# Optimization experiments

Hardware: AMD Instinct MI355X
Metric: run time of the kernel (lower is better)

## Reference

```python
import jax, jax.numpy as jnp
import numpy as np

B, H, S, D = 2, 16, 2048, 128

def setup_inputs() -> dict:
    key = jax.random.key(0)
    kq, kk, kv = jax.random.split(key, 3)
    q = jax.random.normal(kq, (B, H, S, D), dtype=jnp.float32)
    k = jax.random.normal(kk, (B, H, S, D), dtype=jnp.float32)
    v = jax.random.normal(kv, (B, H, S, D), dtype=jnp.float32)
    # causal mask, broadcastable over batch and heads; 0 -> masked out
    mask = jnp.tril(jnp.ones((S, S), dtype=jnp.int32))[None, None, :, :]
    return {"q": q, "k": k, "v": v, "mask": mask}

def reference(q, k, v, mask):
    # scores: [B,H,S,S] -- note: module applies NO 1/sqrt(d) scaling
    attn = jnp.einsum('bhqd,bhkd->bhqk', q, k)
    neg_inf = jnp.finfo(attn.dtype).min
    attn = jnp.where(mask == 0, neg_inf, attn)
    attn = jax.nn.softmax(attn, axis=-1)
    out = jnp.einsum('bhqk,bhkd->bhqd', attn, v)
    return out
```

## Files before the change

kernel.cpp:

```cpp
#include <hip/hip_runtime.h>


#define SQ 2048
#define DH 128
#define BM 64
#define BN 64
#define NELEM 8388608

typedef _Float16 f16x8 __attribute__((ext_vector_type(8)));
typedef float f32x4 __attribute__((ext_vector_type(4)));
typedef unsigned short u16x8 __attribute__((ext_vector_type(8)));

typedef __attribute__((address_space(3))) void lds_t;
typedef __attribute__((address_space(1))) void gmem_t;

__device__ __forceinline__ void gload16(void* lds, const void* g) {
  __builtin_amdgcn_global_load_lds((const gmem_t*)g, (lds_t*)lds, 16, 0, 0);
}

__device__ __forceinline__ unsigned short f2h(float f) {
  return __builtin_bit_cast(unsigned short, (_Float16)f);
}

__global__ __launch_bounds__(256) void prep(const float* __restrict__ k,
                                            const float* __restrict__ v,
                                            unsigned short* __restrict__ ko,
                                            unsigned short* __restrict__ vt) {
  const int tid = threadIdx.x;
  const int bx = blockIdx.x;
  if (bx < 1024) {
    __shared__ unsigned short lv[64 * 132];
    const int bh = bx >> 5;
    const int s0 = (bx & 31) * 64;
    const float* vs = v + ((size_t)bh * SQ + s0) * DH;
    #pragma unroll
    for (int it = 0; it < 8; ++it) {
      int fi = it * 256 + tid;
      int sL = fi >> 5;
      int dL = (fi & 31) * 4;
      float4 val = *(const float4*)(vs + (size_t)sL * DH + dL);
      ushort4 o;
      o.x = f2h(val.x); o.y = f2h(val.y); o.z = f2h(val.z); o.w = f2h(val.w);
      *(ushort4*)(lv + sL * 132 + dL) = o;
    }
    __syncthreads();
    #pragma unroll
    for (int it = 0; it < 4; ++it) {
      int ci = it * 256 + tid;
      int dL = ci >> 3;
      int sg = ci & 7;
      u16x8 o;
      #pragma unroll
      for (int j = 0; j < 8; ++j) o[j] = lv[(sg * 8 + j) * 132 + dL];
      *(u16x8*)(vt + ((size_t)bh * DH + dL) * SQ + s0 + sg * 8) = o;
    }
  } else {
    const int NT = NELEM / 4;
    for (int i = (bx - 1024) * 256 + tid; i < NT; i += 2048 * 256) {
      float4 val = ((const float4*)k)[i];
      ushort4 o;
      o.x = f2h(val.x); o.y = f2h(val.y); o.z = f2h(val.z); o.w = f2h(val.w);
      ((ushort4*)ko)[i] = o;
    }
  }
}

__global__ __launch_bounds__(256, 4) void fattn(const float* __restrict__ Qf,
                                                const unsigned short* __restrict__ Kh,
                                                const unsigned short* __restrict__ Vth,
                                                float* __restrict__ Out) {
  __shared__ char smem[40960];
  const int tid  = threadIdx.x;
  const int wave = tid >> 6;
  const int lane = tid & 63;
  const int quad = lane >> 4;
  const int c    = lane & 15;

  const int t     = (int)blockIdx.x;
  const int xcd   = t & 7;
  const int idx   = t >> 3;
  const int cu    = idx & 31;
  const int round = idx >> 5;
  const int bh    = xcd * 4 + round;
  int qb;
  {
    int b0 = (cu + 8 * (round >> 1)) & 31;
    qb = (round & 1) ? (31 - b0) : b0;
  }
  const int rowbase = qb * BM;

  char* sK = smem;
  char* sV = smem + 16384;
  char* sP = smem + 32768 + wave * 2048;

  const float* Qg = Qf + ((size_t)bh * SQ + rowbase) * DH;
  #pragma unroll
  for (int it = 0; it < 8; ++it) {
    int gi  = it * 256 + tid;
    int row = gi >> 5;
    int sub = gi & 31;
    float4 qv = *(const float4*)(Qg + (size_t)row * DH + sub * 4);
    ushort4 h;
    h.x = f2h(qv.x); h.y = f2h(qv.y); h.z = f2h(qv.z); h.w = f2h(qv.w);
    int gr = (sub >> 1) ^ (row & 7);
    *(ushort4*)(smem + row * 256 + gr * 16 + (sub & 1) * 8) = h;
  }
  __syncthreads();
  f16x8 qf[4];
  {
    int rl = wave * 16 + c;
    #pragma unroll
    for (int ch = 0; ch < 4; ++ch) {
      int gr = (ch * 4 + quad) ^ (c & 7);
      qf[ch] = *(const f16x8*)(smem + rl * 256 + gr * 16);
    }
  }
  __syncthreads();

  f32x4 acc[8];
  #pragma unroll
  for (int dt = 0; dt < 8; ++dt) acc[dt] = (f32x4){0.f, 0.f, 0.f, 0.f};
  float mo = -1e30f, lrow = 0.f;

  const unsigned short* Kbase = Kh + (size_t)bh * SQ * DH;
  const unsigned short* Vbase = Vth + (size_t)bh * DH * SQ;
  const int nkt = qb + 1;

  for (int kt = 0; kt < nkt; ++kt) {
    const int k0 = kt * BN;
    #pragma unroll
    for (int it = 0; it < 4; ++it) {
      int gi  = it * 256 + tid;
      int key = gi >> 4;
      int dg  = (gi & 15) ^ (key & 7);
      gload16(sK + (it * 256 + wave * 64) * 16,
              Kbase + (size_t)(k0 + key) * DH + dg * 8);
    }
    #pragma unroll
    for (int it = 0; it < 4; ++it) {
      int gi = it * 256 + tid;
      int d  = gi >> 3;
      int kg = (gi & 7) ^ (d & 7);
      gload16(sV + (it * 256 + wave * 64) * 16,
              Vbase + (size_t)d * SQ + k0 + kg * 8);
    }
    __syncthreads();

    const bool diag  = (kt == qb);
    const int ntmax  = diag ? wave : 3;
    const int chmax  = diag ? (wave >> 1) : 1;

    f32x4 sc[4];
    #pragma unroll
    for (int nt = 0; nt < 4; ++nt) sc[nt] = (f32x4){0.f, 0.f, 0.f, 0.f};
    #pragma unroll
    for (int nt = 0; nt < 4; ++nt) {
      if (nt <= ntmax) {
        int keyl = nt * 16 + c;
        #pragma unroll
        for (int ch = 0; ch < 4; ++ch) {
          int gr = (ch * 4 + quad) ^ (c & 7);
          f16x8 kf = *(const f16x8*)(sK + keyl * 256 + gr * 16);
          sc[nt] = __builtin_amdgcn_mfma_f32_16x16x32_f16(kf, qf[ch], sc[nt], 0, 0, 0);
        }
      }
    }

    if (diag) {
      int rl = wave * 16 + c;
      #pragma unroll
      for (int nt = 0; nt < 4; ++nt)
        #pragma unroll
        for (int r = 0; r < 4; ++r)
          if (nt * 16 + quad * 4 + r > rl) sc[nt][r] = -1e30f;
    }

    float cm = -1e30f;
    #pragma unroll
    for (int nt = 0; nt < 4; ++nt)
      #pragma unroll
      for (int r = 0; r < 4; ++r) cm = fmaxf(cm, sc[nt][r]);
    cm = fmaxf(cm, __shfl_xor(cm, 16));
    cm = fmaxf(cm, __shfl_xor(cm, 32));
    float mn = fmaxf(mo, cm);
    float al = __expf(mo - mn);
    float rs = 0.f;
    ushort4 pk[4];
    #pragma unroll
    for (int nt = 0; nt < 4; ++nt) {
      #pragma unroll
      for (int r = 0; r < 4; ++r) {
        float p = __expf(sc[nt][r] - mn);
        rs += p;
        ((unsigned short*)&pk[nt])[r] = f2h(p);
      }
    }
    rs += __shfl_xor(rs, 16);
    rs += __shfl_xor(rs, 32);
    lrow = lrow * al + rs;
    mo = mn;
    #pragma unroll
    for (int dt = 0; dt < 8; ++dt) acc[dt] *= al;

    #pragma unroll
    for (int nt = 0; nt < 4; ++nt) {
      int g8 = nt * 2 + (quad >> 1);
      *(ushort4*)(sP + c * 128 + ((g8 ^ (c & 7)) * 16) + (quad & 1) * 8) = pk[nt];
    }

    #pragma unroll
    for (int ch = 0; ch < 2; ++ch) {
      if (ch <= chmax) {
        f16x8 pf = *(const f16x8*)(sP + c * 128 + (((ch * 4 + quad) ^ (c & 7)) * 16));
        #pragma unroll
        for (int dt = 0; dt < 8; ++dt) {
          int d  = dt * 16 + c;
          int gr = (ch * 4 + quad) ^ (c & 7);
          f16x8 vf = *(const f16x8*)(sV + d * 128 + gr * 16);
          acc[dt] = __builtin_amdgcn_mfma_f32_16x16x32_f16(vf, pf, acc[dt], 0, 0, 0);
        }
      }
    }
    __syncthreads();
  }

  const float inv = 1.0f / lrow;
  const int rowg = rowbase + wave * 16 + c;
  float* op = Out + ((size_t)bh * SQ + rowg) * DH;
  #pragma unroll
  for (int dt = 0; dt < 8; ++dt) {
    float4 o;
    o.x = acc[dt][0] * inv;
    o.y = acc[dt][1] * inv;
    o.z = acc[dt][2] * inv;
    o.w = acc[dt][3] * inv;
    *(float4*)(op + dt * 16 + quad * 4) = o;
  }
}

extern "C" void kernel_launch(void* const* d_in, const int* in_sizes, int n_in,
                              void* d_out, int out_size, void* d_ws, size_t ws_size,
                              hipStream_t stream) {
  const float* q = (const float*)d_in[0];
  const float* k = (const float*)d_in[1];
  const float* v = (const float*)d_in[2];
  float* out = (float*)d_out;

  unsigned short* kws = (unsigned short*)d_ws;
  unsigned short* vws = kws + NELEM;

  prep<<<3072, 256, 0, stream>>>(k, v, kws, vws);
  fattn<<<1024, 256, 0, stream>>>(q, kws, vws, out);
}
```

Before: 215.5 us.

## Double-buffer K/V tiles in LDS and raise MFMA wave priority

Splits LDS into two K/V buffers and issues the async global-to-LDS loads for the next key tile before computing on the current one. This removes one barrier per iteration and overlaps load latency with the QK and PV MFMA work. It also wraps the MFMA sections in s_setprio to favour matrix-issuing waves. In exchange LDS per block grows to 72KB and launch bounds drop from 4 to 2 blocks per CU, so there is less cross-block latency hiding.

After: 225.6 us. 4.7% more time.

```diff
diff --git a/kernel.cpp b/kernel.cpp
--- a/kernel.cpp
+++ b/kernel.cpp
@@ -65,11 +65,11 @@
   }
 }
 
-__global__ __launch_bounds__(256, 4) void fattn(const float* __restrict__ Qf,
+__global__ __launch_bounds__(256, 2) void fattn(const float* __restrict__ Qf,
                                                 const unsigned short* __restrict__ Kh,
                                                 const unsigned short* __restrict__ Vth,
                                                 float* __restrict__ Out) {
-  __shared__ char smem[40960];
+  __shared__ char smem[73728];
   const int tid  = threadIdx.x;
   const int wave = tid >> 6;
   const int lane = tid & 63;
@@ -89,9 +89,7 @@
   }
   const int rowbase = qb * BM;
 
-  char* sK = smem;
-  char* sV = smem + 16384;
-  char* sP = smem + 32768 + wave * 2048;
+  char* sP = smem + 65536 + wave * 2048;
 
   const float* Qg = Qf + ((size_t)bh * SQ + rowbase) * DH;
   #pragma unroll
@@ -103,16 +101,32 @@
     ushort4 h;
     h.x = f2h(qv.x); h.y = f2h(qv.y); h.z = f2h(qv.z); h.w = f2h(qv.w);
     int gr = (sub >> 1) ^ (row & 7);
-    *(ushort4*)(smem + row * 256 + gr * 16 + (sub & 1) * 8) = h;
+    *(ushort4*)(smem + 32768 + row * 256 + gr * 16 + (sub & 1) * 8) = h;
   }
   __syncthreads();
+
+  const unsigned short* Kbase = Kh + (size_t)bh * SQ * DH;
+  const unsigned short* Vbase = Vth + (size_t)bh * DH * SQ;
+  const unsigned short* Ksrc = Kbase + (size_t)(tid >> 4) * DH
+                             + ((tid & 15) ^ ((tid >> 4) & 7)) * 8;
+  const unsigned short* Vsrc = Vbase + (size_t)(tid >> 3) * SQ
+                             + ((tid & 7) ^ ((tid >> 3) & 7)) * 8;
+  const int ldsbase = wave * 1024;
+
+  #pragma unroll
+  for (int it = 0; it < 4; ++it)
+    gload16(smem + ldsbase + it * 4096, Ksrc + it * (16 * DH));
+  #pragma unroll
+  for (int it = 0; it < 4; ++it)
+    gload16(smem + 16384 + ldsbase + it * 4096, Vsrc + it * (32 * SQ));
+
   f16x8 qf[4];
   {
     int rl = wave * 16 + c;
     #pragma unroll
     for (int ch = 0; ch < 4; ++ch) {
       int gr = (ch * 4 + quad) ^ (c & 7);
-      qf[ch] = *(const f16x8*)(smem + rl * 256 + gr * 16);
+      qf[ch] = *(const f16x8*)(smem + 32768 + rl * 256 + gr * 16);
     }
   }
   __syncthreads();
@@ -122,29 +136,23 @@
   for (int dt = 0; dt < 8; ++dt) acc[dt] = (f32x4){0.f, 0.f, 0.f, 0.f};
   float mo = -1e30f, lrow = 0.f;
 
-  const unsigned short* Kbase = Kh + (size_t)bh * SQ * DH;
-  const unsigned short* Vbase = Vth + (size_t)bh * DH * SQ;
   const int nkt = qb + 1;
-
+  int cur = 0;
   for (int kt = 0; kt < nkt; ++kt) {
-    const int k0 = kt * BN;
-    #pragma unroll
-    for (int it = 0; it < 4; ++it) {
-      int gi  = it * 256 + tid;
-      int key = gi >> 4;
-      int dg  = (gi & 15) ^ (key & 7);
-      gload16(sK + (it * 256 + wave * 64) * 16,
-              Kbase + (size_t)(k0 + key) * DH + dg * 8);
-    }
-    #pragma unroll
-    for (int it = 0; it < 4; ++it) {
-      int gi = it * 256 + tid;
-      int d  = gi >> 3;
-      int kg = (gi & 7) ^ (d & 7);
-      gload16(sV + (it * 256 + wave * 64) * 16,
-              Vbase + (size_t)d * SQ + k0 + kg * 8);
-    }
-    __syncthreads();
+    char* sK = smem + (cur << 15);
+    char* sV = sK + 16384;
+
+    if (kt + 1 < nkt) {
+      char* nb = smem + ((cur ^ 1) << 15);
+      const unsigned short* Kn = Ksrc + (size_t)(kt + 1) * (BN * DH);
+      const unsigned short* Vn = Vsrc + (size_t)(kt + 1) * BN;
+      #pragma unroll
+      for (int it = 0; it < 4; ++it)
+        gload16(nb + ldsbase + it * 4096, Kn + it * (16 * DH));
+      #pragma unroll
+      for (int it = 0; it < 4; ++it)
+        gload16(nb + 16384 + ldsbase + it * 4096, Vn + it * (32 * SQ));
+    }
 
     const bool diag  = (kt == qb);
     const int ntmax  = diag ? wave : 3;
@@ -153,6 +161,7 @@
     f32x4 sc[4];
     #pragma unroll
     for (int nt = 0; nt < 4; ++nt) sc[nt] = (f32x4){0.f, 0.f, 0.f, 0.f};
+    __builtin_amdgcn_s_setprio(1);
     #pragma unroll
     for (int nt = 0; nt < 4; ++nt) {
       if (nt <= ntmax) {
@@ -165,6 +174,7 @@
         }
       }
     }
+    __builtin_amdgcn_s_setprio(0);
 
     if (diag) {
       int rl = wave * 16 + c;
@@ -208,6 +218,7 @@
       *(ushort4*)(sP + c * 128 + ((g8 ^ (c & 7)) * 16) + (quad & 1) * 8) = pk[nt];
     }
 
+    __builtin_amdgcn_s_setprio(1);
     #pragma unroll
     for (int ch = 0; ch < 2; ++ch) {
       if (ch <= chmax) {
@@ -221,7 +232,10 @@
         }
       }
     }
-    __syncthreads();
+    __builtin_amdgcn_s_setprio(0);
+
+    if (kt + 1 < nkt) __syncthreads();
+    cur ^= 1;
   }
 
   const float inv = 1.0f / lrow;
```
